# Optimization experiments

Measured on AMD Instinct MI355X. Metric: run time of the kernel, lower is better.

## Reference

```python
import jax, jax.numpy as jnp
import numpy as np

WS = 4        # window_size
HEADS = 12    # num_heads


def setup_inputs() -> dict:
    key = jax.random.key(0)
    k1, k2, k3 = jax.random.split(key, 3)
    B, N, E = 32, 4096, 384
    x = jax.random.normal(k1, (B, N, E), dtype=jnp.float32)
    w_in = jax.random.normal(k2, (3 * E, E), dtype=jnp.float32) * 0.02
    b_in = jnp.zeros((3 * E,), dtype=jnp.float32)
    w_out = jax.random.normal(k3, (E, E), dtype=jnp.float32) * 0.02
    b_out = jnp.zeros((E,), dtype=jnp.float32)
    return {"x": x, "w_in": w_in, "b_in": b_in, "w_out": w_out, "b_out": b_out}


def reference(x, w_in, b_in, w_out, b_out):
    B, N, E = x.shape
    H = W = int(np.sqrt(N))
    nh, nw = H // WS, W // WS
    hd = E // HEADS
    T = WS * WS  # tokens per window

    # window partition: [B, H, W, E] -> [B*nh*nw, T, E]
    xw = x.reshape(B, nh, WS, nw, WS, E)
    xw = xw.transpose(0, 1, 3, 2, 4, 5).reshape(-1, T, E)

    # packed QKV projection (torch nn.MultiheadAttention in_proj)
    qkv = xw @ w_in.T + b_in                      # [nWin, T, 3E]
    q, k, v = jnp.split(qkv, 3, axis=-1)          # each [nWin, T, E]

    def split_heads(t):
        return t.reshape(-1, T, HEADS, hd).transpose(0, 2, 1, 3)  # [nWin, h, T, hd]

    q, k, v = split_heads(q), split_heads(k), split_heads(v)
    scale = 1.0 / np.sqrt(hd).astype(np.float32)
    scores = jnp.einsum('whqd,whkd->whqk', q * scale, k)          # [nWin, h, T, T]
    attn = jax.nn.softmax(scores, axis=-1)
    out = jnp.einsum('whqk,whkd->whqd', attn, v)                  # [nWin, h, T, hd]
    out = out.transpose(0, 2, 1, 3).reshape(-1, T, E)
    out = out @ w_out.T + b_out                                   # out_proj

    # window reverse: [B*nh*nw, T, E] -> [B, N, E]
    out = out.reshape(B, nh, nw, WS, WS, E)
    out = out.transpose(0, 1, 3, 2, 4, 5).reshape(B, N, E)
    return out
```

## Files before the change

kernel.cpp:

```cpp
#include <hip/hip_runtime.h>
#include <hip/hip_bf16.h>

typedef __attribute__((ext_vector_type(8))) short short8;
typedef __attribute__((ext_vector_type(4))) float f32x4;

static __device__ __forceinline__ f32x4 MFMA16(short8 a, short8 b, f32x4 c) {
    return __builtin_amdgcn_mfma_f32_16x16x32_bf16(a, b, c, 0, 0, 0);
}
static __device__ __forceinline__ unsigned short f2bf(float f) {
    union { __hip_bfloat16 h; unsigned short u; } c;
    c.h = __float2bfloat16(f);
    return c.u;
}
static __device__ __forceinline__ void gload16(const void* g, void* l) {
    __builtin_amdgcn_global_load_lds(
        (const __attribute__((address_space(1))) unsigned int*)g,
        (__attribute__((address_space(3))) unsigned int*)l, 16, 0, 0);
}

constexpr size_t kWstOff = 0;
constexpr size_t kWosOff = 884736;
constexpr size_t kBrrOff = 1179648;
constexpr size_t kAttOff = 1184256;

__global__ void prep(const float* __restrict__ w_in, const float* __restrict__ b_in,
                     const float* __restrict__ w_out,
                     char* __restrict__ wst, char* __restrict__ wos,
                     float* __restrict__ brr)
{
    const int i = blockIdx.x * 256 + threadIdx.x;
    if (i < 55296) {
        int h = i / 4608, rem = i % 4608;
        int s = rem / 768, t = rem % 768;
        int row = t >> 3, sl = t & 7;
        int c8 = sl ^ (row & 7);
        int sec = row >> 5, d = row & 31;
        int srow = sec * 384 + h * 32 + d;
        int k0 = s * 64 + c8 * 8;
        const float4* src = (const float4*)(w_in + (size_t)srow * 384 + k0);
        float4 a = src[0], b = src[1];
        uint4 w;
        w.x = f2bf(a.x) | ((unsigned)f2bf(a.y) << 16);
        w.y = f2bf(a.z) | ((unsigned)f2bf(a.w) << 16);
        w.z = f2bf(b.x) | ((unsigned)f2bf(b.y) << 16);
        w.w = f2bf(b.z) | ((unsigned)f2bf(b.w) << 16);
        *(uint4*)(wst + (size_t)i * 16) = w;
    } else {
        int j = i - 55296;
        int nb = j / 6144, rem = j % 6144;
        int s = rem / 1024, slot16 = rem % 1024;
        int row = slot16 >> 3, sl = slot16 & 7;
        int c8 = sl ^ (row & 7);
        int srow = nb * 128 + row;
        int k0 = s * 64 + c8 * 8;
        const float4* src = (const float4*)(w_out + (size_t)srow * 384 + k0);
        float4 a = src[0], b = src[1];
        uint4 w;
        w.x = f2bf(a.x) | ((unsigned)f2bf(a.y) << 16);
        w.y = f2bf(a.z) | ((unsigned)f2bf(a.w) << 16);
        w.z = f2bf(b.x) | ((unsigned)f2bf(b.y) << 16);
        w.w = f2bf(b.z) | ((unsigned)f2bf(b.w) << 16);
        *(uint4*)(wos + (size_t)j * 16) = w;
    }
    if (i < 1152) {
        int h = i / 96, jj = i % 96;
        int sec = jj >> 5, d = jj & 31;
        brr[i] = b_in[sec * 384 + h * 32 + d];
    }
}

__global__ void prep_x(const float* __restrict__ x, char* __restrict__ xbf)
{
    const int i = blockIdx.x * 256 + threadIdx.x;
    const int lane = i & 63;
    const int cc = (i >> 6) & 1;
    const int f = (i >> 7) & 7;
    const int rem = i >> 10;
    const int s = rem % 6, mb = rem / 6;

    int T = mb * 128 + f * 16 + (lane & 15);
    int win = T >> 4, t4 = T & 15;
    int bb = win >> 8, wh = (win >> 4) & 15, ww = win & 15;
    int n = (wh * 4 + (t4 >> 2)) * 64 + ww * 4 + (t4 & 3);
    int k0 = s * 64 + cc * 32 + (lane >> 4) * 8;

    const float4* src = (const float4*)(x + ((size_t)bb * 4096 + n) * 384 + k0);
    float4 a = src[0], b = src[1];
    uint4 w;
    w.x = f2bf(a.x) | ((unsigned)f2bf(a.y) << 16);
    w.y = f2bf(a.z) | ((unsigned)f2bf(a.w) << 16);
    w.z = f2bf(b.x) | ((unsigned)f2bf(b.y) << 16);
    w.w = f2bf(b.z) | ((unsigned)f2bf(b.w) << 16);
    *(uint4*)(xbf + (size_t)i * 16) = w;
}

__global__ __launch_bounds__(512, 6)
void qkv_attn(const char* __restrict__ xbf, const char* __restrict__ wst,
              const float* __restrict__ brr, char* __restrict__ attst)
{
    __shared__ __align__(16) char smem[36864];

    const int tid  = threadIdx.x;
    const int lane = tid & 63, wid = tid >> 6;
    const int g = lane >> 4, r16 = lane & 15;

    int b = blockIdx.x;
    int x8 = b & 7, j = b >> 3;
    const int head = j % 12;
    const int mblk = x8 * 128 + j / 12;

    const char* xw = xbf + (size_t)mblk * 98304 + (size_t)wid * 2048 + lane * 16;
    const char* whp = wst + (size_t)head * 73728;

    auto stage_B = [&](int s, int buf) {
        if (tid < 384) {
            char* dst = smem + buf * 12288 + tid * 16;
            const char* src = whp + s * 12288 + tid * 16;
            gload16(src, dst);
            gload16(src + 6144, dst + 6144);
        }
    };

    f32x4 acc[6] = {};
    short8 acur0, acur1, anext0, anext1;

    stage_B(0, 0);
    acur0 = *(const short8*)(xw);
    acur1 = *(const short8*)(xw + 1024);
    stage_B(1, 1);

    #pragma unroll
    for (int s = 0; s < 6; ++s) {
        __builtin_amdgcn_sched_barrier(0);
        if (s < 5 && wid < 6) {
            asm volatile("s_waitcnt vmcnt(2)" ::: "memory");
        } else {
            asm volatile("s_waitcnt vmcnt(0)" ::: "memory");
        }
        __builtin_amdgcn_sched_barrier(0);
        __builtin_amdgcn_s_barrier();
        __builtin_amdgcn_sched_barrier(0);

        if (s < 5) {
            anext0 = *(const short8*)(xw + (s + 1) * 16384);
            anext1 = *(const short8*)(xw + (s + 1) * 16384 + 1024);
        }
        if (s < 4) stage_B(s + 2, (s + 2) % 3);

        const char* bbp = smem + (s % 3) * 12288;
        #pragma unroll
        for (int c = 0; c < 2; ++c) {
            const int sw = ((c * 4 + g) ^ (r16 & 7)) << 4;
            const short8 ac = (c == 0) ? acur0 : acur1;
            #pragma unroll
            for (int nh = 0; nh < 2; ++nh) {
                short8 bf[3];
                #pragma unroll
                for (int k = 0; k < 3; ++k)
                    bf[k] = *(const short8*)(bbp + ((nh * 3 + k) * 16 + r16) * 128 + sw);
                #pragma unroll
                for (int k = 0; k < 3; ++k)
                    acc[nh * 3 + k] = MFMA16(ac, bf[k], acc[nh * 3 + k]);
            }
        }
        acur0 = anext0;
        acur1 = anext1;
    }

    char* tile = smem + wid * 3072;
    #pragma unroll
    for (int ni = 0; ni < 6; ++ni) {
        const int sec = ni >> 1;
        const int d = (ni & 1) * 16 + r16;
        const float bias = brr[head * 96 + ni * 16 + r16];
        float v0 = acc[ni][0] + bias;
        float v1 = acc[ni][1] + bias;
        float v2 = acc[ni][2] + bias;
        float v3 = acc[ni][3] + bias;
        uint2 w;
        w.x = f2bf(v0) | ((unsigned)f2bf(v1) << 16);
        w.y = f2bf(v2) | ((unsigned)f2bf(v3) << 16);
        *(uint2*)(tile + sec * 1024 + d * 32 + g * 8) = w;
    }

    const float kC = 0.17677669529663687f * 1.4426950408889634f;
    const f32x4 zero = {0.f, 0.f, 0.f, 0.f};

    union U8 { unsigned short e[8]; short8 v; };
    U8 ku, qu;
    #pragma unroll
    for (int jj = 0; jj < 8; ++jj) {
        const int off = (g * 8 + jj) * 32 + r16 * 2;
        qu.e[jj] = *(const unsigned short*)(tile + off);
        ku.e[jj] = *(const unsigned short*)(tile + 1024 + off);
    }
    f32x4 s = MFMA16(ku.v, qu.v, zero);

    float m = fmaxf(fmaxf(s[0], s[1]), fmaxf(s[2], s[3]));
    m = fmaxf(m, __shfl_xor(m, 16, 64));
    m = fmaxf(m, __shfl_xor(m, 32, 64));
    float p[4], sum = 0.f;
    #pragma unroll
    for (int r = 0; r < 4; ++r) { p[r] = exp2f((s[r] - m) * kC); sum += p[r]; }
    sum += __shfl_xor(sum, 16, 64);
    sum += __shfl_xor(sum, 32, 64);
    const float inv = 1.f / sum;

    U8 pu;
    pu.e[0] = f2bf(p[0] * inv); pu.e[1] = f2bf(p[1] * inv);
    pu.e[2] = f2bf(p[2] * inv); pu.e[3] = f2bf(p[3] * inv);
    pu.e[4] = 0; pu.e[5] = 0; pu.e[6] = 0; pu.e[7] = 0;

    f32x4 o[2];
    #pragma unroll
    for (int ti = 0; ti < 2; ++ti) {
        U8 vu;
        *(uint2*)&vu.e[0] = *(const uint2*)(tile + 2048 + (ti * 16 + r16) * 32 + g * 8);
        vu.e[4] = 0; vu.e[5] = 0; vu.e[6] = 0; vu.e[7] = 0;
        o[ti] = MFMA16(pu.v, vu.v, zero);
    }

    #pragma unroll
    for (int ti = 0; ti < 2; ++ti)
        #pragma unroll
        for (int r = 0; r < 4; ++r)
            *(unsigned short*)(tile + (g * 4 + r) * 64 + (ti * 16 + r16) * 2)
                = f2bf(o[ti][r]);
    uint4 ov = *(const uint4*)(tile + r16 * 64 + g * 16);

    int row7 = wid * 16 + r16;
    int col8 = head * 4 + g;
    int sst = col8 >> 3;
    int sl = (col8 & 7) ^ (row7 & 7);
    *(uint4*)(attst + (size_t)mblk * 98304 + sst * 16384 + row7 * 128 + sl * 16) = ov;
}

__global__ __launch_bounds__(256, 2)
void out_proj(const char* __restrict__ attst, const char* __restrict__ wos,
              const float* __restrict__ b_out, float* __restrict__ out)
{
    __shared__ __align__(16) char smem[65536];

    const int tid  = threadIdx.x;
    const int lane = tid & 63, wid = tid >> 6;
    const int g = lane >> 4, r16 = lane & 15;
    const int wm = wid >> 1, wn = wid & 1;

    int b = blockIdx.x;
    int L = (b & 7) * 384 + (b >> 3);
    const int mblk = L / 3, nblk = L - mblk * 3;

    auto stage = [&](int s, int buf) {
        const char* asrc = attst + (size_t)mblk * 98304 + s * 16384 + wid * 4096 + lane * 16;
        const char* bsrc = wos   + (size_t)nblk * 98304 + s * 16384 + wid * 4096 + lane * 16;
        char* adst = smem + buf * 16384 + wid * 4096;
        char* bdst = smem + 32768 + buf * 16384 + wid * 4096;
        #pragma unroll
        for (int j = 0; j < 4; ++j) {
            gload16(asrc + j * 1024, adst + j * 1024);
            gload16(bsrc + j * 1024, bdst + j * 1024);
        }
    };

    f32x4 acc[4][4] = {};
    auto compute = [&](int buf) {
        const char* ab = smem + buf * 16384;
        const char* bbp = smem + 32768 + buf * 16384;
        #pragma unroll
        for (int c = 0; c < 2; ++c) {
            const int sw = ((c * 4 + g) ^ (r16 & 7)) << 4;
            short8 a[4], bf[4];
            #pragma unroll
            for (int mi = 0; mi < 4; ++mi)
                a[mi] = *(const short8*)(ab + (wm * 64 + mi * 16 + r16) * 128 + sw);
            #pragma unroll
            for (int ni = 0; ni < 4; ++ni)
                bf[ni] = *(const short8*)(bbp + (wn * 64 + ni * 16 + r16) * 128 + sw);
            #pragma unroll
            for (int mi = 0; mi < 4; ++mi)
                #pragma unroll
                for (int ni = 0; ni < 4; ++ni)
                    acc[mi][ni] = MFMA16(a[mi], bf[ni], acc[mi][ni]);
        }
    };

    stage(0, 0);
    for (int s = 0; s < 6; ++s) {
        __syncthreads();
        if (s < 5) stage(s + 1, (s + 1) & 1);
        compute(s & 1);
    }

    float bias[4];
    #pragma unroll
    for (int ni = 0; ni < 4; ++ni) bias[ni] = b_out[nblk * 128 + wn * 64 + ni * 16 + r16];

    #pragma unroll
    for (int mi = 0; mi < 4; ++mi) {
        #pragma unroll
        for (int r = 0; r < 4; ++r) {
            int T = mblk * 128 + wm * 64 + mi * 16 + g * 4 + r;
            int win = T >> 4, tt = T & 15;
            int bb = win >> 8, wh = (win >> 4) & 15, ww = win & 15;
            size_t o = ((size_t)bb * 4096 + (wh * 4 + (tt >> 2)) * 64 + ww * 4 + (tt & 3)) * 384
                     + nblk * 128 + wn * 64;
            #pragma unroll
            for (int ni = 0; ni < 4; ++ni)
                out[o + ni * 16 + r16] = acc[mi][ni][r] + bias[ni];
        }
    }
}

extern "C" void kernel_launch(void* const* d_in, const int* in_sizes, int n_in,
                              void* d_out, int out_size, void* d_ws, size_t ws_size,
                              hipStream_t stream) {
    const float* x     = (const float*)d_in[0];
    const float* w_in  = (const float*)d_in[1];
    const float* b_in  = (const float*)d_in[2];
    const float* w_out = (const float*)d_in[3];
    const float* b_out = (const float*)d_in[4];
    float* out = (float*)d_out;

    char* ws = (char*)d_ws;
    char*  wst = ws + kWstOff;
    char*  wos = ws + kWosOff;
    float* brr = (float*)(ws + kBrrOff);
    char*  att = ws + kAttOff;
    char*  xbf = (char*)d_out;

    prep<<<dim3(288), dim3(256), 0, stream>>>(w_in, b_in, w_out, wst, wos, brr);
    prep_x<<<dim3(24576), dim3(256), 0, stream>>>(x, xbf);
    qkv_attn<<<dim3(12288), dim3(512), 0, stream>>>(xbf, wst, brr, att);
    out_proj<<<dim3(3072), dim3(256), 0, stream>>>(att, wos, b_out, out);
}
```

Baseline: 272.9 us.

## Use 32x32 MFMA in QKV projection with 4 waves each handling two windows

```diff
diff --git a/kernel.cpp b/kernel.cpp
--- a/kernel.cpp
+++ b/kernel.cpp
@@ -3,9 +3,13 @@
 
 typedef __attribute__((ext_vector_type(8))) short short8;
 typedef __attribute__((ext_vector_type(4))) float f32x4;
+typedef __attribute__((ext_vector_type(16))) float f32x16;
 
 static __device__ __forceinline__ f32x4 MFMA16(short8 a, short8 b, f32x4 c) {
     return __builtin_amdgcn_mfma_f32_16x16x32_bf16(a, b, c, 0, 0, 0);
+}
+static __device__ __forceinline__ f32x16 MFMA32(short8 a, short8 b, f32x16 c) {
+    return __builtin_amdgcn_mfma_f32_32x32x16_bf16(a, b, c, 0, 0, 0);
 }
 static __device__ __forceinline__ unsigned short f2bf(float f) {
     union { __hip_bfloat16 h; unsigned short u; } c;
@@ -94,7 +98,7 @@
     *(uint4*)(xbf + (size_t)i * 16) = w;
 }
 
-__global__ __launch_bounds__(512, 6)
+__global__ __launch_bounds__(256, 4)
 void qkv_attn(const char* __restrict__ xbf, const char* __restrict__ wst,
               const float* __restrict__ brr, char* __restrict__ attst)
 {
@@ -103,136 +107,145 @@
     const int tid  = threadIdx.x;
     const int lane = tid & 63, wid = tid >> 6;
     const int g = lane >> 4, r16 = lane & 15;
+    const int l31 = lane & 31, lh = lane >> 5;
 
     int b = blockIdx.x;
     int x8 = b & 7, j = b >> 3;
     const int head = j % 12;
     const int mblk = x8 * 128 + j / 12;
 
-    const char* xw = xbf + (size_t)mblk * 98304 + (size_t)wid * 2048 + lane * 16;
+    const char* xwA = xbf + (size_t)mblk * 98304
+                    + (size_t)(wid * 2 + ((lane >> 4) & 1)) * 2048 + (lane & 15) * 16;
     const char* whp = wst + (size_t)head * 73728;
 
     auto stage_B = [&](int s, int buf) {
-        if (tid < 384) {
-            char* dst = smem + buf * 12288 + tid * 16;
-            const char* src = whp + s * 12288 + tid * 16;
-            gload16(src, dst);
-            gload16(src + 6144, dst + 6144);
-        }
+        char* dst = smem + buf * 12288 + tid * 16;
+        const char* src = whp + s * 12288 + tid * 16;
+        gload16(src, dst);
+        gload16(src + 4096, dst + 4096);
+        gload16(src + 8192, dst + 8192);
     };
-
-    f32x4 acc[6] = {};
-    short8 acur0, acur1, anext0, anext1;
+    auto loadA = [&](int s, short8* a) {
+        #pragma unroll
+        for (int kk = 0; kk < 4; ++kk)
+            a[kk] = *(const short8*)(xwA + s * 16384 + (kk >> 1) * 1024
+                                     + ((kk & 1) * 2 + lh) * 256);
+    };
+
+    f32x16 acc[3] = {};
+    short8 acur[4], anext[4];
 
     stage_B(0, 0);
-    acur0 = *(const short8*)(xw);
-    acur1 = *(const short8*)(xw + 1024);
+    loadA(0, acur);
     stage_B(1, 1);
 
     #pragma unroll
     for (int s = 0; s < 6; ++s) {
         __builtin_amdgcn_sched_barrier(0);
-        if (s < 5 && wid < 6) {
-            asm volatile("s_waitcnt vmcnt(2)" ::: "memory");
-        } else {
-            asm volatile("s_waitcnt vmcnt(0)" ::: "memory");
-        }
+        if (s < 5) { asm volatile("s_waitcnt vmcnt(3)" ::: "memory"); }
+        else       { asm volatile("s_waitcnt vmcnt(0)" ::: "memory"); }
         __builtin_amdgcn_sched_barrier(0);
         __builtin_amdgcn_s_barrier();
         __builtin_amdgcn_sched_barrier(0);
 
-        if (s < 5) {
-            anext0 = *(const short8*)(xw + (s + 1) * 16384);
-            anext1 = *(const short8*)(xw + (s + 1) * 16384 + 1024);
-        }
+        if (s < 5) loadA(s + 1, anext);
+        __builtin_amdgcn_sched_barrier(0);
         if (s < 4) stage_B(s + 2, (s + 2) % 3);
 
         const char* bbp = smem + (s % 3) * 12288;
         #pragma unroll
-        for (int c = 0; c < 2; ++c) {
-            const int sw = ((c * 4 + g) ^ (r16 & 7)) << 4;
-            const short8 ac = (c == 0) ? acur0 : acur1;
-            #pragma unroll
-            for (int nh = 0; nh < 2; ++nh) {
-                short8 bf[3];
+        for (int kk = 0; kk < 4; ++kk) {
+            #pragma unroll
+            for (int ni = 0; ni < 3; ++ni) {
+                const int row = ni * 32 + l31;
+                short8 bf = *(const short8*)(bbp + row * 128 +
+                                (((kk * 2 + lh) ^ (row & 7)) << 4));
+                acc[ni] = MFMA32(acur[kk], bf, acc[ni]);
+            }
+        }
+        #pragma unroll
+        for (int kk = 0; kk < 4; ++kk) acur[kk] = anext[kk];
+    }
+
+    char* wt0 = smem + (wid * 2) * 3072;
+    char* wt1 = smem + (wid * 2 + 1) * 3072;
+    #pragma unroll
+    for (int ni = 0; ni < 3; ++ni) {
+        const float bias = brr[head * 96 + ni * 32 + l31];
+        #pragma unroll
+        for (int q = 0; q < 4; ++q) {
+            const int rbase = q * 8 + lh * 4;
+            char* tb = (q < 2) ? wt0 : wt1;
+            const int t0 = rbase & 15;
+            if (ni < 2) {
+                const int slot = (((l31 >> 3) ^ ((t0 >> 2) & 3)) << 4) + (l31 & 7) * 2;
                 #pragma unroll
-                for (int k = 0; k < 3; ++k)
-                    bf[k] = *(const short8*)(bbp + ((nh * 3 + k) * 16 + r16) * 128 + sw);
-                #pragma unroll
-                for (int k = 0; k < 3; ++k)
-                    acc[nh * 3 + k] = MFMA16(ac, bf[k], acc[nh * 3 + k]);
+                for (int jj = 0; jj < 4; ++jj)
+                    *(unsigned short*)(tb + ni * 1024 + (t0 + jj) * 64 + slot)
+                        = f2bf(acc[ni][q * 4 + jj] + bias);
+            } else {
+                uint2 w;
+                w.x = f2bf(acc[2][q * 4 + 0] + bias) |
+                      ((unsigned)f2bf(acc[2][q * 4 + 1] + bias) << 16);
+                w.y = f2bf(acc[2][q * 4 + 2] + bias) |
+                      ((unsigned)f2bf(acc[2][q * 4 + 3] + bias) << 16);
+                *(uint2*)(tb + 2048 + l31 * 32 + t0 * 2) = w;
             }
         }
-        acur0 = anext0;
-        acur1 = anext1;
-    }
-
-    char* tile = smem + wid * 3072;
-    #pragma unroll
-    for (int ni = 0; ni < 6; ++ni) {
-        const int sec = ni >> 1;
-        const int d = (ni & 1) * 16 + r16;
-        const float bias = brr[head * 96 + ni * 16 + r16];
-        float v0 = acc[ni][0] + bias;
-        float v1 = acc[ni][1] + bias;
-        float v2 = acc[ni][2] + bias;
-        float v3 = acc[ni][3] + bias;
-        uint2 w;
-        w.x = f2bf(v0) | ((unsigned)f2bf(v1) << 16);
-        w.y = f2bf(v2) | ((unsigned)f2bf(v3) << 16);
-        *(uint2*)(tile + sec * 1024 + d * 32 + g * 8) = w;
     }
 
     const float kC = 0.17677669529663687f * 1.4426950408889634f;
     const f32x4 zero = {0.f, 0.f, 0.f, 0.f};
-
-    union U8 { unsigned short e[8]; short8 v; };
-    U8 ku, qu;
-    #pragma unroll
-    for (int jj = 0; jj < 8; ++jj) {
-        const int off = (g * 8 + jj) * 32 + r16 * 2;
-        qu.e[jj] = *(const unsigned short*)(tile + off);
-        ku.e[jj] = *(const unsigned short*)(tile + 1024 + off);
-    }
-    f32x4 s = MFMA16(ku.v, qu.v, zero);
-
-    float m = fmaxf(fmaxf(s[0], s[1]), fmaxf(s[2], s[3]));
-    m = fmaxf(m, __shfl_xor(m, 16, 64));
-    m = fmaxf(m, __shfl_xor(m, 32, 64));
-    float p[4], sum = 0.f;
-    #pragma unroll
-    for (int r = 0; r < 4; ++r) { p[r] = exp2f((s[r] - m) * kC); sum += p[r]; }
-    sum += __shfl_xor(sum, 16, 64);
-    sum += __shfl_xor(sum, 32, 64);
-    const float inv = 1.f / sum;
-
-    U8 pu;
-    pu.e[0] = f2bf(p[0] * inv); pu.e[1] = f2bf(p[1] * inv);
-    pu.e[2] = f2bf(p[2] * inv); pu.e[3] = f2bf(p[3] * inv);
-    pu.e[4] = 0; pu.e[5] = 0; pu.e[6] = 0; pu.e[7] = 0;
-
-    f32x4 o[2];
-    #pragma unroll
-    for (int ti = 0; ti < 2; ++ti) {
-        U8 vu;
-        *(uint2*)&vu.e[0] = *(const uint2*)(tile + 2048 + (ti * 16 + r16) * 32 + g * 8);
-        vu.e[4] = 0; vu.e[5] = 0; vu.e[6] = 0; vu.e[7] = 0;
-        o[ti] = MFMA16(pu.v, vu.v, zero);
-    }
-
-    #pragma unroll
-    for (int ti = 0; ti < 2; ++ti)
-        #pragma unroll
-        for (int r = 0; r < 4; ++r)
-            *(unsigned short*)(tile + (g * 4 + r) * 64 + (ti * 16 + r16) * 2)
-                = f2bf(o[ti][r]);
-    uint4 ov = *(const uint4*)(tile + r16 * 64 + g * 16);
-
-    int row7 = wid * 16 + r16;
-    int col8 = head * 4 + g;
-    int sst = col8 >> 3;
-    int sl = (col8 & 7) ^ (row7 & 7);
-    *(uint4*)(attst + (size_t)mblk * 98304 + sst * 16384 + row7 * 128 + sl * 16) = ov;
+    const int qsl = ((g ^ ((r16 >> 2) & 3)) << 4);
+
+    #pragma unroll
+    for (int i = 0; i < 2; ++i) {
+        const int win = wid * 2 + i;
+        char* tile = smem + win * 3072;
+
+        short8 qv = *(const short8*)(tile + r16 * 64 + qsl);
+        short8 kv = *(const short8*)(tile + 1024 + r16 * 64 + qsl);
+        f32x4 s = MFMA16(kv, qv, zero);
+
+        float m = fmaxf(fmaxf(s[0], s[1]), fmaxf(s[2], s[3]));
+        m = fmaxf(m, __shfl_xor(m, 16, 64));
+        m = fmaxf(m, __shfl_xor(m, 32, 64));
+        float p[4], sum = 0.f;
+        #pragma unroll
+        for (int r = 0; r < 4; ++r) { p[r] = exp2f((s[r] - m) * kC); sum += p[r]; }
+        sum += __shfl_xor(sum, 16, 64);
+        sum += __shfl_xor(sum, 32, 64);
+        const float inv = 1.f / sum;
+
+        union U8 { unsigned short e[8]; short8 v; };
+        U8 pu;
+        pu.e[0] = f2bf(p[0] * inv); pu.e[1] = f2bf(p[1] * inv);
+        pu.e[2] = f2bf(p[2] * inv); pu.e[3] = f2bf(p[3] * inv);
+        pu.e[4] = 0; pu.e[5] = 0; pu.e[6] = 0; pu.e[7] = 0;
+
+        f32x4 o[2];
+        #pragma unroll
+        for (int ti = 0; ti < 2; ++ti) {
+            U8 vu;
+            *(uint2*)&vu.e[0] = *(const uint2*)(tile + 2048 + (ti * 16 + r16) * 32 + g * 8);
+            vu.e[4] = 0; vu.e[5] = 0; vu.e[6] = 0; vu.e[7] = 0;
+            o[ti] = MFMA16(pu.v, vu.v, zero);
+        }
+
+        #pragma unroll
+        for (int ti = 0; ti < 2; ++ti)
+            #pragma unroll
+            for (int r = 0; r < 4; ++r)
+                *(unsigned short*)(tile + (g * 4 + r) * 64 + (ti * 16 + r16) * 2)
+                    = f2bf(o[ti][r]);
+        uint4 ov = *(const uint4*)(tile + r16 * 64 + g * 16);
+
+        int row7 = win * 16 + r16;
+        int col8 = head * 4 + g;
+        int sst = col8 >> 3;
+        int sl = (col8 & 7) ^ (row7 & 7);
+        *(uint4*)(attst + (size_t)mblk * 98304 + sst * 16384 + row7 * 128 + sl * 16) = ov;
+    }
 }
 
 __global__ __launch_bounds__(256, 2)
@@ -330,6 +343,6 @@
 
     prep<<<dim3(288), dim3(256), 0, stream>>>(w_in, b_in, w_out, wst, wos, brr);
     prep_x<<<dim3(24576), dim3(256), 0, stream>>>(x, xbf);
-    qkv_attn<<<dim3(12288), dim3(512), 0, stream>>>(xbf, wst, brr, att);
+    qkv_attn<<<dim3(12288), dim3(256), 0, stream>>>(xbf, wst, brr, att);
     out_proj<<<dim3(3072), dim3(256), 0, stream>>>(att, wos, b_out, out);
 }
```

After: 275.8 us. About the same (+1.0%).
